# Kernel optimization log

Hardware: AMD Instinct MI355X
Metric: run time of the kernel (lower is better)

The kernel has to match this reference:

```python
import jax, jax.numpy as jnp
import numpy as np

B, S, D, H = 4, 2048, 1024, 16
DK = D // H

def setup_inputs() -> dict:
    key = jax.random.key(0)
    ks = jax.random.split(key, 5)
    scale = D ** -0.5  # keep activations well-scaled for random weights
    return {
        "x": jax.random.normal(ks[0], (B, S, D), dtype=jnp.float32),
        "w_q": jax.random.normal(ks[1], (D, D), dtype=jnp.float32) * scale,
        "w_k": jax.random.normal(ks[2], (D, D), dtype=jnp.float32) * scale,
        "w_v": jax.random.normal(ks[3], (D, D), dtype=jnp.float32) * scale,
        "w_o": jax.random.normal(ks[4], (D, D), dtype=jnp.float32) * scale,
        "b_o": jnp.zeros((D,), dtype=jnp.float32),
    }

def reference(x, w_q, w_k, w_v, w_o, b_o):
    b, s, d = x.shape
    # nn.Linear applies x @ W^T; project then split heads -> [b, h, s, dk]
    q = (x @ w_q.T).reshape(b, s, H, DK).transpose(0, 2, 1, 3)
    k = (x @ w_k.T).reshape(b, s, H, DK).transpose(0, 2, 1, 3)
    v = (x @ w_v.T).reshape(b, s, H, DK).transpose(0, 2, 1, 3)
    scores = jnp.einsum('bhqd,bhkd->bhqk', q, k) * (DK ** -0.5)
    causal = jnp.tril(jnp.ones((s, s), dtype=bool))  # [s, s]
    scores = jnp.where(causal, scores, jnp.float32(-1e9))
    attn = jax.nn.softmax(scores, axis=-1)
    out = jnp.einsum('bhqk,bhkd->bhqd', attn, v)
    out = out.transpose(0, 2, 1, 3).reshape(b, s, d)
    return out @ w_o.T + b_o
```

## Files before the change

### kernel.cpp

```cpp
#include <hip/hip_runtime.h>

typedef unsigned short u16;
typedef unsigned int u32;
typedef __attribute__((ext_vector_type(4))) u16 u16x4;
typedef __attribute__((ext_vector_type(8))) short short8;
typedef __attribute__((ext_vector_type(4))) float f32x4;
typedef __attribute__((ext_vector_type(16))) float f32x16;
typedef __attribute__((ext_vector_type(4))) u32 uint4v;

#define AS1 __attribute__((address_space(1)))
#define AS3 __attribute__((address_space(3)))

#define B_  4
#define S_  2048
#define D_  1024
#define H_  16
#define DK_ 64

#define WAIT_VM(n) asm volatile("s_waitcnt vmcnt(" #n ")" ::: "memory")
#define WAIT_LGK0  asm volatile("s_waitcnt lgkmcnt(0)" ::: "memory")

__device__ __forceinline__ u16 f2bf(float f) {
  union { float f; unsigned u; } v; v.f = f;
  unsigned r = v.u + 0x7fffu + ((v.u >> 16) & 1u);
  return (u16)(r >> 16);
}

__device__ __forceinline__ u32 cvt_pk_bf16(float lo, float hi) {
  u32 r;
  asm("v_cvt_pk_bf16_f32 %0, %1, %2" : "=v"(r) : "v"(lo), "v"(hi));
  return r;
}

__device__ __forceinline__ void pl32_swap(u32& a, u32& b) {
  asm("v_permlane32_swap_b32 %0, %1" : "+v"(a), "+v"(b));
}

__device__ __forceinline__ void gload_lds16(const void* g, void* l) {
  __builtin_amdgcn_global_load_lds((const AS1 void*)g, (AS3 void*)l, 16, 0, 0);
}

__global__ __launch_bounds__(256) void conv_bf16(const float* __restrict__ in,
                                                 u16* __restrict__ out,
                                                 int n, float scale) {
  int i = (blockIdx.x * 256 + threadIdx.x) * 8;
  if (i >= n) return;
  f32x4 a = *reinterpret_cast<const f32x4*>(in + i);
  f32x4 b = *reinterpret_cast<const f32x4*>(in + i + 4);
  union { u16 u[8]; uint4v v; } r;
#pragma unroll
  for (int j = 0; j < 4; ++j) {
    r.u[j]     = f2bf(a[j] * scale);
    r.u[4 + j] = f2bf(b[j] * scale);
  }
  *reinterpret_cast<uint4v*>(out + i) = r.v;
}

__global__ __launch_bounds__(256) void conv_w4(const float* __restrict__ w0,
                                               const float* __restrict__ w1,
                                               const float* __restrict__ w2,
                                               const float* __restrict__ w3,
                                               u16* __restrict__ out, float s0) {
  int y = blockIdx.y;
  const float* src = (y == 0) ? w0 : (y == 1) ? w1 : (y == 2) ? w2 : w3;
  float scale = (y == 0) ? s0 : 1.0f;
  int i = (blockIdx.x * 256 + threadIdx.x) * 8;
  f32x4 a = *reinterpret_cast<const f32x4*>(src + i);
  f32x4 b = *reinterpret_cast<const f32x4*>(src + i + 4);
  union { u16 u[8]; uint4v v; } r;
#pragma unroll
  for (int j = 0; j < 4; ++j) {
    r.u[j]     = f2bf(a[j] * scale);
    r.u[4 + j] = f2bf(b[j] * scale);
  }
  *reinterpret_cast<uint4v*>(out + (size_t)y * (D_ * D_) + i) = r.v;
}

template<int MODE>
__global__ __launch_bounds__(256) void gemm_bt(const u16* __restrict__ A,
                                               const u16* __restrict__ B,
                                               u16* __restrict__ Qb,
                                               u16* __restrict__ Kb,
                                               u16* __restrict__ Vt,
                                               float* __restrict__ Cf,
                                               const float* __restrict__ bias,
                                               int M, int N, int K, int nbx) {
  __shared__ __attribute__((aligned(16))) u16 As[128 * 64];
  __shared__ __attribute__((aligned(16))) u16 Bs[128 * 64];

  const int t = threadIdx.x;
  const int l = t & 63;
  const int w = t >> 6;
  const int wr = w >> 1, wc = w & 1;
  const int dd = blockIdx.x;
  const int cpx = gridDim.x >> 3;
  const int lid = (dd & 7) * cpx + (dd >> 3);
  const int m0 = (lid / nbx) * 128;
  const int n0 = (lid % nbx) * 128;

  f32x4 zero = {0.f, 0.f, 0.f, 0.f};
  f32x4 acc[4][4];
#pragma unroll
  for (int i = 0; i < 4; ++i)
#pragma unroll
    for (int j = 0; j < 4; ++j) acc[i][j] = zero;

  for (int k0 = 0; k0 < K; k0 += 64) {
    __syncthreads();
#pragma unroll
    for (int i = 0; i < 4; ++i) {
      int slot = i * 256 + t;
      int r = slot >> 3, c = slot & 7;
      const u16* srcA = A + (size_t)(m0 + r) * K + k0 + ((c ^ (r & 7)) * 8);
      gload_lds16(srcA, (char*)As + (size_t)(i * 256 + w * 64) * 16);
      const u16* srcB = B + (size_t)(n0 + r) * K + k0 + ((c ^ (r & 7)) * 8);
      gload_lds16(srcB, (char*)Bs + (size_t)(i * 256 + w * 64) * 16);
    }
    __syncthreads();

#pragma unroll
    for (int kc = 0; kc < 2; ++kc) {
      short8 a[4], bf[4];
      int lc = kc * 4 + (l >> 4);
#pragma unroll
      for (int i = 0; i < 4; ++i) {
        int ra = wr * 64 + i * 16 + (l & 15);
        a[i] = *reinterpret_cast<const short8*>(&As[ra * 64 + ((lc ^ (ra & 7)) * 8)]);
        int rb = wc * 64 + i * 16 + (l & 15);
        bf[i] = *reinterpret_cast<const short8*>(&Bs[rb * 64 + ((lc ^ (rb & 7)) * 8)]);
      }
#pragma unroll
      for (int mi = 0; mi < 4; ++mi)
#pragma unroll
        for (int ni = 0; ni < 4; ++ni)
          acc[mi][ni] = __builtin_amdgcn_mfma_f32_16x16x32_bf16(a[mi], bf[ni], acc[mi][ni], 0, 0, 0);
    }
  }

#pragma unroll
  for (int ni = 0; ni < 4; ++ni) {
    int col = n0 + wc * 64 + ni * 16 + (l & 15);
    float bv = (MODE == 1) ? bias[col] : 0.f;
#pragma unroll
    for (int mi = 0; mi < 4; ++mi) {
      int row0 = m0 + wr * 64 + mi * 16 + (l >> 4) * 4;
      if (MODE == 1) {
#pragma unroll
        for (int r = 0; r < 4; ++r)
          Cf[(size_t)(row0 + r) * N + col] = acc[mi][ni][r] + bv;
      } else {
        if (col < 2048) {
          u16* dst = (col < 1024) ? Qb : Kb;
          int c = col & 1023;
#pragma unroll
          for (int r = 0; r < 4; ++r)
            dst[(size_t)(row0 + r) * 1024 + c] = f2bf(acc[mi][ni][r]);
        } else {
          int vc = col - 2048;
          int bh = (row0 >> 11) * 16 + (vc >> 6);
          int s0 = row0 & 2047;
          u16x4 pk;
#pragma unroll
          for (int r = 0; r < 4; ++r) pk[r] = f2bf(acc[mi][ni][r]);
          *reinterpret_cast<u16x4*>(Vt + ((size_t)(bh * 64 + (vc & 63))) * 2048 + s0) = pk;
        }
      }
    }
  }
}

__global__ __launch_bounds__(512) void attn_fwd(const u16* __restrict__ Q,
                                                const u16* __restrict__ K,
                                                const u16* __restrict__ Vtg,
                                                u16* __restrict__ AO) {
  __shared__ __attribute__((aligned(16))) u16 smem[24576];
  u16* Ksb = smem;
  u16* Vsb = smem + 12288;

  const int t = threadIdx.x;
  const int l = t & 63;
  const int w = t >> 6;
  const int hi = l >> 5;
  const int hi8 = hi * 8, hi4 = hi * 4;
  const int bh = blockIdx.x;
  const int by = blockIdx.y;
  const int s = (by < 4) ? (7 - 2 * by) : (2 * (by - 4));
  const size_t qkbase = (size_t)((bh >> 4) * S_) * D_ + (bh & 15) * DK_;
  const u16* Vg = Vtg + (size_t)bh * 64 * S_;

  const int qw = s * 256 + w * 32;
  const int qi = qw + (l & 31);

  short8 qf[4];
#pragma unroll
  for (int c = 0; c < 4; ++c)
    qf[c] = *reinterpret_cast<const short8*>(Q + qkbase + (size_t)qi * D_ + c * 16 + hi8);

  f32x16 o0 = {0,0,0,0,0,0,0,0,0,0,0,0,0,0,0,0};
  f32x16 o1 = {0,0,0,0,0,0,0,0,0,0,0,0,0,0,0,0};
  float l_r = 0.f;

  const int nst = 4 * (s + 1);

  auto stage = [&](int jt, u16* kdst, u16* vdst) {
    const u16* Ksrc = K + qkbase + (size_t)(jt * 64) * D_;
    const u16* Vsrc = Vg + jt * 64;
    int r = t >> 3, c = t & 7;
    gload_lds16(Ksrc + (size_t)r * D_ + ((c ^ (r & 7)) * 8),
                (char*)kdst + (size_t)t * 16);
    gload_lds16(Vsrc + (size_t)r * S_ + ((c ^ (r & 7)) * 8),
                (char*)vdst + (size_t)t * 16);
  };

  stage(0, Ksb, Vsb);
  stage(1, Ksb + 4096, Vsb + 4096);
  stage(2, Ksb + 8192, Vsb + 8192);
  int o0b = 0, o1b = 4096, o2b = 8192;

  for (int it = 0; it < nst; ++it) {
    if (it < nst - 2)       { WAIT_VM(4); }
    else if (it == nst - 2) { WAIT_VM(2); }
    else                    { WAIT_VM(0); }
    __builtin_amdgcn_s_barrier();
    __builtin_amdgcn_sched_barrier(0);

    const int j0 = it * 64;
    u16* ks = Ksb + o0b;
    u16* vs = Vsb + o0b;

    if (j0 <= qw + 31) {
      f32x16 s0 = {0,0,0,0,0,0,0,0,0,0,0,0,0,0,0,0};
      f32x16 s1 = {0,0,0,0,0,0,0,0,0,0,0,0,0,0,0,0};
#pragma unroll
      for (int c = 0; c < 4; ++c) {
        int cl = 2 * c + hi;
        int k0r = l & 31, k1r = (l & 31) + 32;
        short8 kf0 = *reinterpret_cast<const short8*>(&ks[k0r * 64 + ((cl ^ (k0r & 7)) * 8)]);
        short8 kf1 = *reinterpret_cast<const short8*>(&ks[k1r * 64 + ((cl ^ (k1r & 7)) * 8)]);
        s0 = __builtin_amdgcn_mfma_f32_32x32x16_bf16(kf0, qf[c], s0, 0, 0, 0);
        s1 = __builtin_amdgcn_mfma_f32_32x32x16_bf16(kf1, qf[c], s1, 0, 0, 0);
      }
      if (j0 + 63 > qw) {
#pragma unroll
        for (int r = 0; r < 16; ++r) {
          int key = j0 + (r & 3) + 8 * (r >> 2) + hi4;
          if (key > qi) s0[r] = -INFINITY;
          if (key + 32 > qi) s1[r] = -INFINITY;
        }
      }
      {
        float sum = 0.f;
#pragma unroll
        for (int r = 0; r < 16; ++r) { s0[r] = exp2f(s0[r]); sum += s0[r]; }
#pragma unroll
        for (int r = 0; r < 16; ++r) { s1[r] = exp2f(s1[r]); sum += s1[r]; }
        sum += __shfl_xor(sum, 32);
        l_r += sum;
      }
#pragma unroll
      for (int ksl = 0; ksl < 4; ++ksl) {
        const int b = 8 * (ksl & 1);
        const f32x16& ps = (ksl < 2) ? s0 : s1;
        u32 c0 = cvt_pk_bf16(ps[b + 0], ps[b + 1]);
        u32 c1 = cvt_pk_bf16(ps[b + 2], ps[b + 3]);
        u32 c2 = cvt_pk_bf16(ps[b + 4], ps[b + 5]);
        u32 c3 = cvt_pk_bf16(ps[b + 6], ps[b + 7]);
        pl32_swap(c0, c2);
        pl32_swap(c1, c3);
        union { u32 u[4]; short8 s; } pa;
        pa.u[0] = c0; pa.u[1] = c1; pa.u[2] = c2; pa.u[3] = c3;
        int cl = 2 * ksl + hi;
        int d0r = l & 31, d1r = (l & 31) + 32;
        short8 vf0 = *reinterpret_cast<const short8*>(&vs[d0r * 64 + ((cl ^ (d0r & 7)) * 8)]);
        short8 vf1 = *reinterpret_cast<const short8*>(&vs[d1r * 64 + ((cl ^ (d1r & 7)) * 8)]);
        o0 = __builtin_amdgcn_mfma_f32_32x32x16_bf16(vf0, pa.s, o0, 0, 0, 0);
        o1 = __builtin_amdgcn_mfma_f32_32x32x16_bf16(vf1, pa.s, o1, 0, 0, 0);
      }
    }

    WAIT_LGK0;
    __builtin_amdgcn_sched_barrier(0);
    __builtin_amdgcn_s_barrier();
    if (it + 3 < nst) stage(it + 3, Ksb + o0b, Vsb + o0b);
    int tmp = o0b; o0b = o1b; o1b = o2b; o2b = tmp;
  }

  float inv = 1.0f / l_r;
  u16* Ob = smem + w * 2304;
#pragma unroll
  for (int acc = 0; acc < 2; ++acc) {
    const f32x16& oo = acc ? o1 : o0;
#pragma unroll
    for (int rp = 0; rp < 8; ++rp) {
      u32 pk = cvt_pk_bf16(oo[2 * rp] * inv, oo[2 * rp + 1] * inv);
      int d0 = ((2 * rp) & 3) + 8 * (rp >> 1) + hi4 + 32 * acc;
      *reinterpret_cast<u32*>(&Ob[(l & 31) * 72 + d0]) = pk;
    }
  }
  __syncthreads();
  int qq = l >> 1;
  int chb = (l & 1) * 4;
#pragma unroll
  for (int c2 = 0; c2 < 4; ++c2) {
    uint4v vv = *reinterpret_cast<const uint4v*>(&Ob[qq * 72 + (chb + c2) * 8]);
    *reinterpret_cast<uint4v*>(&AO[qkbase + (size_t)(qw + qq) * D_ + (chb + c2) * 8]) = vv;
  }
}

extern "C" void kernel_launch(void* const* d_in, const int* in_sizes, int n_in,
                              void* d_out, int out_size, void* d_ws, size_t ws_size,
                              hipStream_t stream) {
  const float* x  = (const float*)d_in[0];
  const float* wq = (const float*)d_in[1];
  const float* wk = (const float*)d_in[2];
  const float* wv = (const float*)d_in[3];
  const float* wo = (const float*)d_in[4];
  const float* bo = (const float*)d_in[5];
  float* out = (float*)d_out;

  char* ws = (char*)d_ws;
  u16* XB   = (u16*)(ws);
  u16* WQKV = (u16*)(ws + (size_t)(16 << 20));
  u16* WOB  = (u16*)(ws + (size_t)(22 << 20));
  u16* Qb   = (u16*)(ws + (size_t)(24 << 20));
  u16* Kb   = (u16*)(ws + (size_t)(40 << 20));
  u16* Vt   = (u16*)(ws + (size_t)(56 << 20));
  u16* AO   = (u16*)(ws + (size_t)(72 << 20));

  const int nx = B_ * S_ * D_;
  const int nw = D_ * D_;

  conv_bf16<<<nx / 2048, 256, 0, stream>>>(x, XB, nx, 1.0f);
  conv_w4<<<dim3(nw / 2048, 4), 256, 0, stream>>>(wq, wk, wv, wo, WQKV,
                                                  0.18033688011112042f);

  gemm_bt<0><<<1536, 256, 0, stream>>>(
      XB, WQKV, Qb, Kb, Vt, nullptr, nullptr, B_ * S_, 3072, D_, 24);

  attn_fwd<<<dim3(B_ * H_, 8), 512, 0, stream>>>(Qb, Kb, Vt, AO);

  gemm_bt<1><<<512, 256, 0, stream>>>(
      AO, WOB, nullptr, nullptr, nullptr, out, bo, B_ * S_, D_, D_, 8);
}
```

Baseline: 171.3 us.

## Double-buffer LDS tiles in projection GEMM to overlap loads with MFMA

Splits the GEMM shared-memory tiles into two buffers and prefetches the next two K tiles with direct global-to-LDS loads, so the loads are in flight while MFMAs run on the current buffer. Explicit vmcnt waits and raw s_barrier calls replace the two __syncthreads per iteration. This doubles LDS use per block (64 KB), which may reduce occupancy, and relies on the hand-counted vmcnt being correct.

```diff
diff --git a/kernel.cpp b/kernel.cpp
--- a/kernel.cpp
+++ b/kernel.cpp
@@ -85,8 +85,8 @@
                                                float* __restrict__ Cf,
                                                const float* __restrict__ bias,
                                                int M, int N, int K, int nbx) {
-  __shared__ __attribute__((aligned(16))) u16 As[128 * 64];
-  __shared__ __attribute__((aligned(16))) u16 Bs[128 * 64];
+  __shared__ __attribute__((aligned(16))) u16 As[2][128 * 64];
+  __shared__ __attribute__((aligned(16))) u16 Bs[2][128 * 64];
 
   const int t = threadIdx.x;
   const int l = t & 63;
@@ -97,6 +97,7 @@
   const int lid = (dd & 7) * cpx + (dd >> 3);
   const int m0 = (lid / nbx) * 128;
   const int n0 = (lid % nbx) * 128;
+  const int NT = K >> 6;
 
   f32x4 zero = {0.f, 0.f, 0.f, 0.f};
   f32x4 acc[4][4];
@@ -105,18 +106,26 @@
 #pragma unroll
     for (int j = 0; j < 4; ++j) acc[i][j] = zero;
 
-  for (int k0 = 0; k0 < K; k0 += 64) {
-    __syncthreads();
+  auto stage = [&](int kt, int buf) {
 #pragma unroll
     for (int i = 0; i < 4; ++i) {
       int slot = i * 256 + t;
       int r = slot >> 3, c = slot & 7;
-      const u16* srcA = A + (size_t)(m0 + r) * K + k0 + ((c ^ (r & 7)) * 8);
-      gload_lds16(srcA, (char*)As + (size_t)(i * 256 + w * 64) * 16);
-      const u16* srcB = B + (size_t)(n0 + r) * K + k0 + ((c ^ (r & 7)) * 8);
-      gload_lds16(srcB, (char*)Bs + (size_t)(i * 256 + w * 64) * 16);
-    }
-    __syncthreads();
+      gload_lds16(A + (size_t)(m0 + r) * K + kt * 64 + ((c ^ (r & 7)) * 8),
+                  (char*)&As[buf][0] + (size_t)(i * 256 + w * 64) * 16);
+      gload_lds16(B + (size_t)(n0 + r) * K + kt * 64 + ((c ^ (r & 7)) * 8),
+                  (char*)&Bs[buf][0] + (size_t)(i * 256 + w * 64) * 16);
+    }
+  };
+
+  stage(0, 0);
+  stage(1, 1);
+
+  for (int kt = 0; kt < NT; ++kt) {
+    const int buf = kt & 1;
+    if (kt < NT - 1) { WAIT_VM(8); } else { WAIT_VM(0); }
+    __builtin_amdgcn_s_barrier();
+    __builtin_amdgcn_sched_barrier(0);
 
 #pragma unroll
     for (int kc = 0; kc < 2; ++kc) {
@@ -125,9 +134,9 @@
 #pragma unroll
       for (int i = 0; i < 4; ++i) {
         int ra = wr * 64 + i * 16 + (l & 15);
-        a[i] = *reinterpret_cast<const short8*>(&As[ra * 64 + ((lc ^ (ra & 7)) * 8)]);
+        a[i] = *reinterpret_cast<const short8*>(&As[buf][ra * 64 + ((lc ^ (ra & 7)) * 8)]);
         int rb = wc * 64 + i * 16 + (l & 15);
-        bf[i] = *reinterpret_cast<const short8*>(&Bs[rb * 64 + ((lc ^ (rb & 7)) * 8)]);
+        bf[i] = *reinterpret_cast<const short8*>(&Bs[buf][rb * 64 + ((lc ^ (rb & 7)) * 8)]);
       }
 #pragma unroll
       for (int mi = 0; mi < 4; ++mi)
@@ -135,6 +144,11 @@
         for (int ni = 0; ni < 4; ++ni)
           acc[mi][ni] = __builtin_amdgcn_mfma_f32_16x16x32_bf16(a[mi], bf[ni], acc[mi][ni], 0, 0, 0);
     }
+
+    WAIT_LGK0;
+    __builtin_amdgcn_sched_barrier(0);
+    __builtin_amdgcn_s_barrier();
+    if (kt + 2 < NT) stage(kt + 2, buf);
   }
 
 #pragma unroll
```

Result: faster. 163.3 us (-4.7%).
